# Kernel tuning notes

Measured on AMD Instinct MI355X. Metric: run time of the kernel, lower is better.

## Reference

```python
import jax, jax.numpy as jnp
import numpy as np

N_NODES = 20000
IN_CH = 512
HEADS = 8
CH = 64  # hidden_layer per head
E = 320000
E_LABEL = 100000


def setup_inputs() -> dict:
    key = jax.random.key(0)
    ks = jax.random.split(key, 8)
    x = jax.random.normal(ks[0], (N_NODES, IN_CH), dtype=jnp.float32)
    edge_index = jax.random.randint(ks[1], (2, E), 0, N_NODES)
    edge_label_index = jax.random.randint(ks[2], (2, E_LABEL), 0, N_NODES)
    # GATv2Conv params (share_weights=False, bias=True)
    sc = 1.0 / np.sqrt(IN_CH)
    W_l = jax.random.normal(ks[3], (IN_CH, HEADS * CH), dtype=jnp.float32) * sc
    W_r = jax.random.normal(ks[4], (IN_CH, HEADS * CH), dtype=jnp.float32) * sc
    att = jax.random.normal(ks[5], (HEADS, CH), dtype=jnp.float32) * (1.0 / np.sqrt(CH))
    bias = jnp.zeros((HEADS * CH,), dtype=jnp.float32)
    gamma = jnp.ones((HEADS * CH,), dtype=jnp.float32)
    beta = jnp.zeros((HEADS * CH,), dtype=jnp.float32)
    return {"x": x, "edge_index": edge_index, "edge_label_index": edge_label_index,
            "W_l": W_l, "W_r": W_r, "att": att, "bias": bias,
            "gamma": gamma, "beta": beta}


def reference(x, edge_index, edge_label_index, W_l, W_r, att, bias, gamma, beta):
    N = x.shape[0]
    H, C = att.shape
    src, dst = edge_index[0], edge_index[1]
    # GATv2Conv: separate source/target linear maps
    xl = (x @ W_l).reshape(N, H, C)
    xr = (x @ W_r).reshape(N, H, C)
    # per-edge attention logits (GATv2: leaky_relu BEFORE attention vector)
    e = jax.nn.leaky_relu(xl[src] + xr[dst], negative_slope=0.2)  # [E,H,C]
    alpha = jnp.einsum('ehc,hc->eh', e, att)                      # [E,H]
    # softmax over incoming edges of each destination node
    amax = jax.ops.segment_max(alpha, dst, num_segments=N)        # [N,H]
    alpha = jnp.exp(alpha - amax[dst])
    denom = jax.ops.segment_sum(alpha, dst, num_segments=N)       # [N,H]
    alpha = alpha / (denom[dst] + 1e-16)
    # scatter-add aggregation of attended source messages
    out = jax.ops.segment_sum(alpha[:, :, None] * xl[src], dst, num_segments=N)  # [N,H,C]
    out = out.reshape(N, H * C) + bias
    # BatchNorm1d (training-mode batch stats, eps=1e-5)
    mu = out.mean(axis=0)
    var = out.var(axis=0)
    out = (out - mu) * jax.lax.rsqrt(var + 1e-5) * gamma + beta
    out = jax.nn.relu(out)  # dropout is identity in deterministic reference
    # gather + dot-product link scoring
    s = out[edge_label_index[0]]
    t = out[edge_label_index[1]]
    return jnp.sum(s * t, axis=1)  # [E_LABEL]
```

## Files before the change

### kernel.cpp

```cpp
#include <hip/hip_runtime.h>
#include <hip/hip_bf16.h>
#include <cstdint>

#define IN_CH 512
#define HC    512
#define HEADS 8
#define NPACK 1024

typedef __attribute__((ext_vector_type(8))) short bf16x8;
typedef __attribute__((ext_vector_type(8))) ushort u16x8;
typedef __attribute__((ext_vector_type(4))) float f32x4;
typedef __attribute__((ext_vector_type(2))) float f32x2;
typedef const __attribute__((address_space(1))) uint8_t* gaddr_t;
typedef __attribute__((address_space(3))) uint8_t* laddr_t;

__device__ inline ushort f2bf(float f) {
  uint32_t u = __float_as_uint(f);
  return (ushort)((u + 0x7fffu + ((u >> 16) & 1u)) >> 16);
}
__device__ inline float bf2f(ushort u) {
  return __uint_as_float(((uint32_t)u) << 16);
}

#if defined(__has_builtin)
#if __has_builtin(__builtin_amdgcn_cvt_pk_f32_fp8) && __has_builtin(__builtin_amdgcn_cvt_pk_fp8_f32)
#define HAVE_HW_FP8 1
#endif
#if __has_builtin(__builtin_elementwise_max)
#define HAVE_EW_MAX 1
#endif
#endif

__device__ __forceinline__ float fp8_decode_sw(uint32_t v) {
  const uint32_t t = v & 0x7fu;
  float m;
  if (t >= 8u) m = __uint_as_float((((t >> 3) + 120u) << 23) | ((t & 7u) << 20));
  else m = (float)t * 0.001953125f;
  return (v & 0x80u) ? -m : m;
}
__device__ __forceinline__ uint8_t fp8_encode_sw(float f) {
  const uint32_t b = __float_as_uint(f);
  const uint32_t s = (b >> 24) & 0x80u;
  uint32_t a = b & 0x7fffffffu;
  if (a >= 0x43e00000u) return (uint8_t)(s | 0x7eu);
  if (a < 0x3c800000u) {
    const int qi = (int)(__uint_as_float(a) * 512.0f + 0.5f);
    return (uint8_t)(s | (qi >= 8 ? 8u : (uint32_t)qi));
  }
  const uint32_t r = a + 0x7ffffu + ((a >> 20) & 1u);
  const uint32_t e = r >> 23;
  if (e > 135u) return (uint8_t)(s | 0x7eu);
  return (uint8_t)(s | ((e - 120u) << 3) | ((r >> 20) & 7u));
}

template<bool HI>
__device__ __forceinline__ f32x2 fp8x2_dec(uint32_t u) {
#ifdef HAVE_HW_FP8
  return __builtin_amdgcn_cvt_pk_f32_fp8(u, HI);
#else
  const uint32_t w = HI ? (u >> 16) : u;
  f32x2 r;
  r.x = fp8_decode_sw(w & 0xffu);
  r.y = fp8_decode_sw((w >> 8) & 0xffu);
  return r;
#endif
}
__device__ __forceinline__ uint8_t f32_to_fp8(float f) {
#ifdef HAVE_HW_FP8
  return (uint8_t)(__builtin_amdgcn_cvt_pk_fp8_f32(f, f, 0, false) & 0xff);
#else
  return fp8_encode_sw(f);
#endif
}
__device__ __forceinline__ uint32_t fp8x4_pack(f32x2 a, f32x2 b) {
#ifdef HAVE_HW_FP8
  uint32_t w = __builtin_amdgcn_cvt_pk_fp8_f32(a.x, a.y, 0, false);
  w = __builtin_amdgcn_cvt_pk_fp8_f32(b.x, b.y, w, true);
  return w;
#else
  return (uint32_t)fp8_encode_sw(a.x) | ((uint32_t)fp8_encode_sw(a.y) << 8) |
         ((uint32_t)fp8_encode_sw(b.x) << 16) | ((uint32_t)fp8_encode_sw(b.y) << 24);
#endif
}

__device__ __forceinline__ f32x2 pk_max(f32x2 a, f32x2 b) {
#ifdef HAVE_EW_MAX
  return __builtin_elementwise_max(a, b);
#else
  f32x2 r; r.x = fmaxf(a.x, b.x); r.y = fmaxf(a.y, b.y); return r;
#endif
}

template<int CTRL>
__device__ __forceinline__ float dpp_add(float s) {
  const int t = __builtin_amdgcn_update_dpp(0, __float_as_int(s), CTRL, 0xf, 0xf, true);
  return s + __int_as_float(t);
}

__global__ void prep(const float* __restrict__ x, ushort* __restrict__ xb,
                     const float* __restrict__ Wl, const float* __restrict__ Wr,
                     ushort* __restrict__ bt,
                     const int* __restrict__ ei, int* __restrict__ counts,
                     const int* __restrict__ eli, int* __restrict__ counts2,
                     int n4, int E, int EL, int nbc, int nbp, int nbh) {
  const int b = blockIdx.x;
  if (b < nbc) {
    const int i = b * 256 + threadIdx.x;
    if (i < n4) {
      const float4 v = ((const float4*)x)[i];
      ushort4 o;
      o.x = f2bf(v.x); o.y = f2bf(v.y); o.z = f2bf(v.z); o.w = f2bf(v.w);
      ((ushort4*)xb)[i] = o;
    }
  } else if (b < nbc + nbp) {
    const int i = (b - nbc) * 256 + threadIdx.x;
    if (i < NPACK * IN_CH) {
      const int n = i >> 9, k = i & 511;
      const float v = (n < HC) ? Wl[(size_t)k * HC + n] : Wr[(size_t)k * HC + (n - HC)];
      bt[i] = f2bf(v);
    }
  } else if (b < nbc + nbp + nbh) {
    const int e = (b - nbc - nbp) * 256 + threadIdx.x;
    if (e < E) atomicAdd(&counts[ei[E + e]], 1);
  } else {
    const int e = (b - nbc - nbp - nbh) * 256 + threadIdx.x;
    if (e < EL) atomicAdd(&counts2[eli[e]], 1);
  }
}

__global__ __launch_bounds__(512) void gemm_mfma(
    const ushort* __restrict__ xb, const ushort* __restrict__ bt,
    uint8_t* __restrict__ xl8, ushort* __restrict__ xrb, int M) {
  __shared__ __align__(16) ushort As[3][256 * 32];
  __shared__ __align__(16) ushort Bs[3][128 * 32];
  const int sw  = (blockIdx.x & 7) * 79 + (blockIdx.x >> 3);
  const int row0 = (sw >> 3) * 256;
  const int col0 = (sw & 7) * 128;
  const int wave = threadIdx.x >> 6, lane = threadIdx.x & 63;
  const int quad = lane >> 4, m16 = lane & 15;
  const int wrow = (wave >> 1) * 64;
  const int wcol = (wave & 1) * 64;
  const int srow = lane >> 2;
  const int scol = (lane & 3) * 8;
  const f32x4 zero = {0.f, 0.f, 0.f, 0.f};
  f32x4 acc[4][4];
  #pragma unroll
  for (int i = 0; i < 4; ++i)
    #pragma unroll
    for (int j = 0; j < 4; ++j) acc[i][j] = zero;

  auto stage = [&](int buf, int kt) {
    const int k0 = kt * 32;
    const int r = wave * 16 + srow;
    const ushort* ga0 = xb + (size_t)(row0 + r) * IN_CH + k0 + scol;
    __builtin_amdgcn_global_load_lds((gaddr_t)ga0, (laddr_t)(&As[buf][(wave * 16) * 32]), 16, 0, 0);
    const ushort* ga1 = xb + (size_t)(row0 + 128 + r) * IN_CH + k0 + scol;
    __builtin_amdgcn_global_load_lds((gaddr_t)ga1, (laddr_t)(&As[buf][(128 + wave * 16) * 32]), 16, 0, 0);
    const ushort* gb = bt + (size_t)(col0 + r) * IN_CH + k0 + scol;
    __builtin_amdgcn_global_load_lds((gaddr_t)gb, (laddr_t)(&Bs[buf][(wave * 16) * 32]), 16, 0, 0);
  };
  auto compute = [&](int buf) {
    bf16x8 af[4], bfr[4];
    #pragma unroll
    for (int i = 0; i < 4; ++i)
      af[i] = *(const bf16x8*)(&As[buf][(wrow + i * 16 + m16) * 32 + quad * 8]);
    #pragma unroll
    for (int j = 0; j < 4; ++j)
      bfr[j] = *(const bf16x8*)(&Bs[buf][(wcol + j * 16 + m16) * 32 + quad * 8]);
    #pragma unroll
    for (int i = 0; i < 4; ++i)
      #pragma unroll
      for (int j = 0; j < 4; ++j)
        acc[i][j] = __builtin_amdgcn_mfma_f32_16x16x32_bf16(af[i], bfr[j], acc[i][j], 0, 0, 0);
  };

  stage(0, 0);
  stage(1, 1);
  int buf = 0;
  for (int kt = 0; kt <= 13; ++kt) {
    asm volatile("s_waitcnt vmcnt(3)" ::: "memory");
    __builtin_amdgcn_s_barrier();
    int nbuf = buf + 2; if (nbuf >= 3) nbuf -= 3;
    stage(nbuf, kt + 2);
    compute(buf);
    ++buf; if (buf == 3) buf = 0;
  }
  asm volatile("s_waitcnt vmcnt(3)" ::: "memory");
  __builtin_amdgcn_s_barrier();
  compute(buf);
  ++buf; if (buf == 3) buf = 0;
  asm volatile("s_waitcnt vmcnt(0)" ::: "memory");
  __builtin_amdgcn_s_barrier();
  compute(buf);

  const bool isL = (col0 < HC);
  if (isL) {
    #pragma unroll
    for (int i = 0; i < 4; ++i) {
      const int r = row0 + wrow + i * 16 + quad * 4;
      #pragma unroll
      for (int j = 0; j < 4; ++j) {
        const int cg = col0 + wcol + j * 16 + m16;
        #pragma unroll
        for (int t = 0; t < 4; ++t) {
          const int rr = r + t;
          if (rr < M) xl8[(size_t)rr * HC + cg] = f32_to_fp8(acc[i][j][t]);
        }
      }
    }
  } else {
    const int cbase = col0 - HC;
    #pragma unroll
    for (int i = 0; i < 4; ++i) {
      const int r = row0 + wrow + i * 16 + quad * 4;
      #pragma unroll
      for (int j = 0; j < 4; ++j) {
        const int cg = cbase + wcol + j * 16 + m16;
        #pragma unroll
        for (int t = 0; t < 4; ++t) {
          const int rr = r + t;
          if (rr < M) xrb[(size_t)rr * HC + cg] = f2bf(acc[i][j][t]);
        }
      }
    }
  }
}

__global__ __launch_bounds__(256) void scan_fused(
    const int* __restrict__ cA, int* __restrict__ oA, int* __restrict__ curA,
    int* __restrict__ fA,
    const int* __restrict__ cB, int* __restrict__ oB, int* __restrict__ curB,
    int* __restrict__ fB, int Nn, int nb) {
  const int half = (blockIdx.x >= nb) ? 1 : 0;
  const int blk  = blockIdx.x - half * nb;
  const int* counts = half ? cB : cA;
  int* offsets = half ? oB : oA;
  int* cursor  = half ? curB : curA;
  int* flags   = half ? fB : fA;
  __shared__ int tmp[256];
  __shared__ int sPref;
  const int t = threadIdx.x;
  const int i = blk * 256 + t;
  const int v = (i < Nn) ? counts[i] : 0;
  tmp[t] = v;
  __syncthreads();
  for (int d = 1; d < 256; d <<= 1) {
    int add = (t >= d) ? tmp[t - d] : 0;
    __syncthreads();
    tmp[t] += add;
    __syncthreads();
  }
  if (t == 0) atomicExch(&flags[blk], tmp[255] + 1);
  if (t < 64) {
    int s = 0;
    for (int b = t; b < blk; b += 64) {
      int f;
      do { f = atomicOr(&flags[b], 0); } while (f == 0);
      s += f - 1;
    }
    #pragma unroll
    for (int off = 32; off > 0; off >>= 1) s += __shfl_down(s, off, 64);
    if (t == 0) sPref = s;
  }
  __syncthreads();
  const int pref = sPref;
  if (i < Nn) {
    const int o = tmp[t] - v + pref;
    offsets[i] = o;
    cursor[i] = o;
  }
}

__global__ void csr_fill(const int* __restrict__ ei, int* __restrict__ cursor,
                         int* __restrict__ csr_src,
                         const int* __restrict__ eli, int* __restrict__ cursor2,
                         int2* __restrict__ csr_te, int E, int EL, int nbE) {
  const int b = blockIdx.x;
  if (b < nbE) {
    const int e = b * 256 + threadIdx.x;
    if (e < E) {
      const int pos = atomicAdd(&cursor[ei[E + e]], 1);
      csr_src[pos] = ei[e];
    }
  } else {
    const int e = (b - nbE) * 256 + threadIdx.x;
    if (e < EL) {
      const int pos = atomicAdd(&cursor2[eli[e]], 1);
      csr_te[pos] = make_int2(eli[EL + e], e);
    }
  }
}

__global__ __launch_bounds__(256) void gatv2_agg(
    const uint8_t* __restrict__ xl8, const ushort* xrb, const float* __restrict__ att,
    const int* __restrict__ offsets, const int* __restrict__ counts,
    const int* __restrict__ csr_src, uint8_t* __restrict__ agg8, int Nn) {
  const int node = blockIdx.x * 4 + (threadIdx.x >> 6);
  const int lane = threadIdx.x & 63;
  if (node >= Nn) return;
  const int start = offsets[node];
  const int deg   = counts[node];
  uint2* pd = (uint2*)(agg8 + (size_t)node * HC + lane * 8);
  if (deg == 0) {
    const uint2 z = {0u, 0u};
    *pd = z;
    return;
  }
  f32x2 rv2[4], tv2[4];
  {
    const u16x8 ur = *(const u16x8*)(xrb + (size_t)node * HC + lane * 8);
    #pragma unroll
    for (int c = 0; c < 4; ++c) {
      rv2[c].x = bf2f((ushort)ur[2 * c]);
      rv2[c].y = bf2f((ushort)ur[2 * c + 1]);
    }
    const float4* pa = (const float4*)(att + lane * 8);
    const float4 t0 = pa[0], t1 = pa[1];
    tv2[0].x = t0.x; tv2[0].y = t0.y;
    tv2[1].x = t0.z; tv2[1].y = t0.w;
    tv2[2].x = t1.x; tv2[2].y = t1.y;
    tv2[3].x = t1.z; tv2[3].y = t1.w;
  }
  f32x2 acc2[4] = {{0.f, 0.f}, {0.f, 0.f}, {0.f, 0.f}, {0.f, 0.f}};
  float densum = 0.f;
  const int* ps = csr_src + start;
  auto row = [&](int idx) {
    return *(const uint2*)(xl8 + (size_t)ps[idx] * HC + lane * 8);
  };
  auto body = [&](const uint2 cur) {
    f32x2 a0 = fp8x2_dec<false>(cur.x);
    f32x2 a1 = fp8x2_dec<true>(cur.x);
    f32x2 a2 = fp8x2_dec<false>(cur.y);
    f32x2 a3 = fp8x2_dec<true>(cur.y);
    f32x2 v, s2;
    v = a0 + rv2[0]; s2  = pk_max(v, 0.2f * v) * tv2[0];
    v = a1 + rv2[1]; s2 += pk_max(v, 0.2f * v) * tv2[1];
    v = a2 + rv2[2]; s2 += pk_max(v, 0.2f * v) * tv2[2];
    v = a3 + rv2[3]; s2 += pk_max(v, 0.2f * v) * tv2[3];
    float s = s2.x + s2.y;
    s = dpp_add<0xB1>(s);
    s = dpp_add<0x4E>(s);
    s = dpp_add<0x141>(s);
    const float ea = __expf(s);
    densum += ea;
    const f32x2 eav = {ea, ea};
    acc2[0] += eav * a0;
    acc2[1] += eav * a1;
    acc2[2] += eav * a2;
    acc2[3] += eav * a3;
  };

  uint2 b0 = {}, b1 = {};
  b0 = row(0);
  if (deg > 1) b1 = row(1);
  int i = 0;
  for (; i + 2 <= deg; i += 2) {
    const uint2 c0 = b0;
    if (i + 2 < deg) b0 = row(i + 2);
    const uint2 c1 = b1;
    if (i + 3 < deg) b1 = row(i + 3);
    body(c0);
    body(c1);
  }
  if (i < deg) body(b0);

  const float inv = 1.0f / (densum + 1e-16f);
  const f32x2 iv = {inv, inv};
  uint2 pack;
  pack.x = fp8x4_pack(acc2[0] * iv, acc2[1] * iv);
  pack.y = fp8x4_pack(acc2[2] * iv, acc2[3] * iv);
  *pd = pack;
}

__global__ void bn_stats(const uint8_t* __restrict__ agg8, float* __restrict__ gsum,
                         float* __restrict__ gsq, int* __restrict__ ctr,
                         const float* __restrict__ gamma, const float* __restrict__ beta,
                         float* __restrict__ aScale, float* __restrict__ bShift,
                         float invN, int Nn) {
  const int t = threadIdx.x;
  const int rows_per_block = (Nn + gridDim.x - 1) / gridDim.x;
  const int r0 = blockIdx.x * rows_per_block;
  const int r1 = min(Nn, r0 + rows_per_block);
  float s0 = 0.f, s1 = 0.f, q0 = 0.f, q1 = 0.f;
  for (int r = r0; r < r1; ++r) {
    const uchar2 u = ((const uchar2*)(agg8 + (size_t)r * HC))[t];
    const f32x2 v = fp8x2_dec<false>((uint32_t)u.x | ((uint32_t)u.y << 8));
    s0 += v.x; q0 += v.x * v.x;
    s1 += v.y; q1 += v.y * v.y;
  }
  atomicAdd(&gsum[2 * t], s0);
  atomicAdd(&gsum[2 * t + 1], s1);
  atomicAdd(&gsq[2 * t], q0);
  atomicAdd(&gsq[2 * t + 1], q1);
  __shared__ int isLast;
  __syncthreads();
  if (t == 0) {
    __threadfence();
    isLast = (atomicAdd(ctr, 1) == (int)gridDim.x - 1) ? 1 : 0;
  }
  __syncthreads();
  if (isLast) {
    #pragma unroll
    for (int k = 0; k < 2; ++k) {
      const int c = t + k * 256;
      const float sum = atomicAdd(&gsum[c], 0.0f);
      const float sq  = atomicAdd(&gsq[c], 0.0f);
      const float m = sum * invN;
      const float var = sq * invN - m * m;
      const float rs = rsqrtf(var + 1e-5f);
      const float a = rs * gamma[c];
      aScale[c] = a;
      bShift[c] = beta[c] - m * a;
    }
  }
}

__global__ __launch_bounds__(256) void score_g(
    const uint8_t* __restrict__ agg8, const float* __restrict__ aScale,
    const float* __restrict__ bShift, const int* __restrict__ off2,
    const int* __restrict__ cnt2, const int2* __restrict__ csr_te,
    float* __restrict__ out, int Nn) {
  const int node = blockIdx.x * 4 + (threadIdx.x >> 6);
  const int lane = threadIdx.x & 63;
  if (node >= Nn) return;
  const int start = off2[node];
  const int deg   = cnt2[node];
  if (deg == 0) return;
  const f32x2 z2 = {0.f, 0.f};
  f32x2 aS2[4], bS2[4], ys2[4];
  {
    const float4* pa = (const float4*)(aScale + lane * 8);
    const float4 a0 = pa[0], a1 = pa[1];
    aS2[0].x=a0.x; aS2[0].y=a0.y; aS2[1].x=a0.z; aS2[1].y=a0.w;
    aS2[2].x=a1.x; aS2[2].y=a1.y; aS2[3].x=a1.z; aS2[3].y=a1.w;
    const float4* pb = (const float4*)(bShift + lane * 8);
    const float4 c0 = pb[0], c1 = pb[1];
    bS2[0].x=c0.x; bS2[0].y=c0.y; bS2[1].x=c0.z; bS2[1].y=c0.w;
    bS2[2].x=c1.x; bS2[2].y=c1.y; bS2[3].x=c1.z; bS2[3].y=c1.w;
    const uint2 us = *(const uint2*)(agg8 + (size_t)node * HC + lane * 8);
    ys2[0] = pk_max(z2, fp8x2_dec<false>(us.x) * aS2[0] + bS2[0]);
    ys2[1] = pk_max(z2, fp8x2_dec<true>(us.x)  * aS2[1] + bS2[1]);
    ys2[2] = pk_max(z2, fp8x2_dec<false>(us.y) * aS2[2] + bS2[2]);
    ys2[3] = pk_max(z2, fp8x2_dec<true>(us.y)  * aS2[3] + bS2[3]);
  }
  const int2* pte = csr_te + start;
  auto row = [&](int idx) {
    return *(const uint2*)(agg8 + (size_t)pte[idx].x * HC + lane * 8);
  };
  auto emit = [&](const uint2 ut, int eid) {
    f32x2 s2;
    s2  = ys2[0] * pk_max(z2, fp8x2_dec<false>(ut.x) * aS2[0] + bS2[0]);
    s2 += ys2[1] * pk_max(z2, fp8x2_dec<true>(ut.x)  * aS2[1] + bS2[1]);
    s2 += ys2[2] * pk_max(z2, fp8x2_dec<false>(ut.y) * aS2[2] + bS2[2]);
    s2 += ys2[3] * pk_max(z2, fp8x2_dec<true>(ut.y)  * aS2[3] + bS2[3]);
    float s = s2.x + s2.y;
    s = dpp_add<0xB1>(s);
    s = dpp_add<0x4E>(s);
    s = dpp_add<0x141>(s);
    s = dpp_add<0x140>(s);
    s = dpp_add<0x142>(s);
    s = dpp_add<0x143>(s);
    if (lane == 63) out[eid] = s;
  };
  uint2 b0 = {}, b1 = {};
  b0 = row(0);
  if (deg > 1) b1 = row(1);
  int j = 0;
  for (; j + 2 <= deg; j += 2) {
    const uint2 c0 = b0;
    if (j + 2 < deg) b0 = row(j + 2);
    const uint2 c1 = b1;
    if (j + 3 < deg) b1 = row(j + 3);
    emit(c0, pte[j].y);
    emit(c1, pte[j + 1].y);
  }
  if (j < deg) emit(b0, pte[j].y);
}

extern "C" void kernel_launch(void* const* d_in, const int* in_sizes, int n_in,
                              void* d_out, int out_size, void* d_ws, size_t ws_size,
                              hipStream_t stream) {
  const float* x     = (const float*)d_in[0];
  const int*   ei    = (const int*)d_in[1];
  const int*   eli   = (const int*)d_in[2];
  const float* W_l   = (const float*)d_in[3];
  const float* W_r   = (const float*)d_in[4];
  const float* att   = (const float*)d_in[5];
  const float* gamma = (const float*)d_in[7];
  const float* beta  = (const float*)d_in[8];
  float* out = (float*)d_out;

  const int Nn = in_sizes[0] / IN_CH;
  const int E  = in_sizes[1] / 2;
  const int EL = in_sizes[2] / 2;

  uint8_t* xl8 = (uint8_t*)d_ws;
  ushort* xrb = (ushort*)d_ws + (size_t)Nn * HC;
  ushort* xbf = xrb + (size_t)Nn * HC;
  ushort* btb = xbf + (size_t)Nn * IN_CH;
  int* counts   = (int*)(btb + (size_t)NPACK * IN_CH);
  int* counts2  = counts + Nn;
  float* gsum   = (float*)(counts2 + Nn);
  float* gsq    = gsum + HC;
  int* flagsA   = (int*)(gsq + HC);
  int* flagsB   = flagsA + 128;
  int* bnctr    = flagsB + 128;
  int* offsets  = bnctr + 64;
  int* cursor   = offsets + Nn;
  int* offsets2 = cursor + Nn;
  int* cursor2  = offsets2 + Nn;
  int* csr_src  = cursor2 + Nn;
  int2* csr_te  = (int2*)(csr_src + E);
  float* aScale = (float*)(csr_te + EL);
  float* bShift = aScale + HC;
  uint8_t* agg8 = (uint8_t*)xbf;

  const int nb  = (Nn + 255) / 256;
  const int nbc = (Nn * IN_CH / 4 + 255) / 256;
  const int nbp = (NPACK * IN_CH + 255) / 256;
  const int nbh = (E + 255) / 256;
  const int nbh2 = (EL + 255) / 256;

  (void)hipMemsetAsync(counts, 0, (2 * (size_t)Nn + 2 * HC + 320) * sizeof(int), stream);

  prep<<<nbc + nbp + nbh + nbh2, 256, 0, stream>>>(
      x, xbf, W_l, W_r, btb, ei, counts, eli, counts2,
      Nn * IN_CH / 4, E, EL, nbc, nbp, nbh);

  gemm_mfma<<<632, 512, 0, stream>>>(xbf, btb, xl8, xrb, Nn);

  scan_fused<<<2 * nb, 256, 0, stream>>>(counts, offsets, cursor, flagsA,
                                         counts2, offsets2, cursor2, flagsB, Nn, nb);
  csr_fill<<<nbh + nbh2, 256, 0, stream>>>(ei, cursor, csr_src,
                                           eli, cursor2, csr_te, E, EL, nbh);

  gatv2_agg<<<(Nn + 3) / 4, 256, 0, stream>>>(xl8, xrb, att, offsets, counts,
                                              csr_src, agg8, Nn);

  bn_stats<<<200, 256, 0, stream>>>(agg8, gsum, gsq, bnctr, gamma, beta,
                                    aScale, bShift, 1.0f / (float)Nn, Nn);

  score_g<<<(Nn + 3) / 4, 256, 0, stream>>>(agg8, aScale, bShift, offsets2,
                                            counts2, csr_te, out, Nn);
}
```

Measured before the change: 271.2 us.

## Fuse BatchNorm statistics accumulation into GATv2 aggregation kernel

Removes the separate bn_stats launch and computes per-channel sum and sum-of-squares inside gatv2_agg. Each block reduces its four nodes into shared memory with atomics, then issues 1024 global float atomics, and a last-block counter finalizes the scale and shift. This saves one kernel launch and a reread of agg8. In exchange it adds about 5000 blocks each doing 1024 global atomics on the same 1024 addresses, which can create heavy contention. It also changes the statistics to use the unquantized values rather than the fp8-decoded ones.

```diff
diff --git a/kernel.cpp b/kernel.cpp
--- a/kernel.cpp
+++ b/kernel.cpp
@@ -294,107 +294,115 @@
 __global__ __launch_bounds__(256) void gatv2_agg(
     const uint8_t* __restrict__ xl8, const ushort* xrb, const float* __restrict__ att,
     const int* __restrict__ offsets, const int* __restrict__ counts,
-    const int* __restrict__ csr_src, uint8_t* __restrict__ agg8, int Nn) {
+    const int* __restrict__ csr_src, uint8_t* __restrict__ agg8,
+    float* __restrict__ gsum, float* __restrict__ gsq, int* __restrict__ ctr,
+    const float* __restrict__ gamma, const float* __restrict__ beta,
+    float* __restrict__ aScale, float* __restrict__ bShift, float invN, int Nn) {
+  __shared__ float sSum[HC];
+  __shared__ float sSq[HC];
   const int node = blockIdx.x * 4 + (threadIdx.x >> 6);
   const int lane = threadIdx.x & 63;
-  if (node >= Nn) return;
-  const int start = offsets[node];
-  const int deg   = counts[node];
-  uint2* pd = (uint2*)(agg8 + (size_t)node * HC + lane * 8);
-  if (deg == 0) {
-    const uint2 z = {0u, 0u};
-    *pd = z;
-    return;
-  }
-  f32x2 rv2[4], tv2[4];
-  {
-    const u16x8 ur = *(const u16x8*)(xrb + (size_t)node * HC + lane * 8);
-    #pragma unroll
-    for (int c = 0; c < 4; ++c) {
-      rv2[c].x = bf2f((ushort)ur[2 * c]);
-      rv2[c].y = bf2f((ushort)ur[2 * c + 1]);
-    }
-    const float4* pa = (const float4*)(att + lane * 8);
-    const float4 t0 = pa[0], t1 = pa[1];
-    tv2[0].x = t0.x; tv2[0].y = t0.y;
-    tv2[1].x = t0.z; tv2[1].y = t0.w;
-    tv2[2].x = t1.x; tv2[2].y = t1.y;
-    tv2[3].x = t1.z; tv2[3].y = t1.w;
-  }
-  f32x2 acc2[4] = {{0.f, 0.f}, {0.f, 0.f}, {0.f, 0.f}, {0.f, 0.f}};
-  float densum = 0.f;
-  const int* ps = csr_src + start;
-  auto row = [&](int idx) {
-    return *(const uint2*)(xl8 + (size_t)ps[idx] * HC + lane * 8);
-  };
-  auto body = [&](const uint2 cur) {
-    f32x2 a0 = fp8x2_dec<false>(cur.x);
-    f32x2 a1 = fp8x2_dec<true>(cur.x);
-    f32x2 a2 = fp8x2_dec<false>(cur.y);
-    f32x2 a3 = fp8x2_dec<true>(cur.y);
-    f32x2 v, s2;
-    v = a0 + rv2[0]; s2  = pk_max(v, 0.2f * v) * tv2[0];
-    v = a1 + rv2[1]; s2 += pk_max(v, 0.2f * v) * tv2[1];
-    v = a2 + rv2[2]; s2 += pk_max(v, 0.2f * v) * tv2[2];
-    v = a3 + rv2[3]; s2 += pk_max(v, 0.2f * v) * tv2[3];
-    float s = s2.x + s2.y;
-    s = dpp_add<0xB1>(s);
-    s = dpp_add<0x4E>(s);
-    s = dpp_add<0x141>(s);
-    const float ea = __expf(s);
-    densum += ea;
-    const f32x2 eav = {ea, ea};
-    acc2[0] += eav * a0;
-    acc2[1] += eav * a1;
-    acc2[2] += eav * a2;
-    acc2[3] += eav * a3;
-  };
-
-  uint2 b0 = {}, b1 = {};
-  b0 = row(0);
-  if (deg > 1) b1 = row(1);
-  int i = 0;
-  for (; i + 2 <= deg; i += 2) {
-    const uint2 c0 = b0;
-    if (i + 2 < deg) b0 = row(i + 2);
-    const uint2 c1 = b1;
-    if (i + 3 < deg) b1 = row(i + 3);
-    body(c0);
-    body(c1);
-  }
-  if (i < deg) body(b0);
-
-  const float inv = 1.0f / (densum + 1e-16f);
-  const f32x2 iv = {inv, inv};
-  uint2 pack;
-  pack.x = fp8x4_pack(acc2[0] * iv, acc2[1] * iv);
-  pack.y = fp8x4_pack(acc2[2] * iv, acc2[3] * iv);
-  *pd = pack;
-}
-
-__global__ void bn_stats(const uint8_t* __restrict__ agg8, float* __restrict__ gsum,
-                         float* __restrict__ gsq, int* __restrict__ ctr,
-                         const float* __restrict__ gamma, const float* __restrict__ beta,
-                         float* __restrict__ aScale, float* __restrict__ bShift,
-                         float invN, int Nn) {
-  const int t = threadIdx.x;
-  const int rows_per_block = (Nn + gridDim.x - 1) / gridDim.x;
-  const int r0 = blockIdx.x * rows_per_block;
-  const int r1 = min(Nn, r0 + rows_per_block);
-  float s0 = 0.f, s1 = 0.f, q0 = 0.f, q1 = 0.f;
-  for (int r = r0; r < r1; ++r) {
-    const uchar2 u = ((const uchar2*)(agg8 + (size_t)r * HC))[t];
-    const f32x2 v = fp8x2_dec<false>((uint32_t)u.x | ((uint32_t)u.y << 8));
-    s0 += v.x; q0 += v.x * v.x;
-    s1 += v.y; q1 += v.y * v.y;
-  }
-  atomicAdd(&gsum[2 * t], s0);
-  atomicAdd(&gsum[2 * t + 1], s1);
-  atomicAdd(&gsq[2 * t], q0);
-  atomicAdd(&gsq[2 * t + 1], q1);
+  const int tid  = threadIdx.x;
+  sSum[tid] = 0.f; sSum[tid + 256] = 0.f;
+  sSq[tid]  = 0.f; sSq[tid + 256]  = 0.f;
+
+  f32x2 v2[4] = {{0.f, 0.f}, {0.f, 0.f}, {0.f, 0.f}, {0.f, 0.f}};
+  const bool active = (node < Nn);
+  if (active) {
+    const int start = offsets[node];
+    const int deg   = counts[node];
+    uint2* pd = (uint2*)(agg8 + (size_t)node * HC + lane * 8);
+    if (deg == 0) {
+      const uint2 z = {0u, 0u};
+      *pd = z;
+    } else {
+      f32x2 rv2[4], tv2[4];
+      {
+        const u16x8 ur = *(const u16x8*)(xrb + (size_t)node * HC + lane * 8);
+        #pragma unroll
+        for (int c = 0; c < 4; ++c) {
+          rv2[c].x = bf2f((ushort)ur[2 * c]);
+          rv2[c].y = bf2f((ushort)ur[2 * c + 1]);
+        }
+        const float4* pa = (const float4*)(att + lane * 8);
+        const float4 t0 = pa[0], t1 = pa[1];
+        tv2[0].x = t0.x; tv2[0].y = t0.y;
+        tv2[1].x = t0.z; tv2[1].y = t0.w;
+        tv2[2].x = t1.x; tv2[2].y = t1.y;
+        tv2[3].x = t1.z; tv2[3].y = t1.w;
+      }
+      f32x2 acc2[4] = {{0.f, 0.f}, {0.f, 0.f}, {0.f, 0.f}, {0.f, 0.f}};
+      float densum = 0.f;
+      const int* ps = csr_src + start;
+      auto row = [&](int idx) {
+        return *(const uint2*)(xl8 + (size_t)ps[idx] * HC + lane * 8);
+      };
+      auto body = [&](const uint2 cur) {
+        f32x2 a0 = fp8x2_dec<false>(cur.x);
+        f32x2 a1 = fp8x2_dec<true>(cur.x);
+        f32x2 a2 = fp8x2_dec<false>(cur.y);
+        f32x2 a3 = fp8x2_dec<true>(cur.y);
+        f32x2 v, s2;
+        v = a0 + rv2[0]; s2  = pk_max(v, 0.2f * v) * tv2[0];
+        v = a1 + rv2[1]; s2 += pk_max(v, 0.2f * v) * tv2[1];
+        v = a2 + rv2[2]; s2 += pk_max(v, 0.2f * v) * tv2[2];
+        v = a3 + rv2[3]; s2 += pk_max(v, 0.2f * v) * tv2[3];
+        float s = s2.x + s2.y;
+        s = dpp_add<0xB1>(s);
+        s = dpp_add<0x4E>(s);
+        s = dpp_add<0x141>(s);
+        const float ea = __expf(s);
+        densum += ea;
+        const f32x2 eav = {ea, ea};
+        acc2[0] += eav * a0;
+        acc2[1] += eav * a1;
+        acc2[2] += eav * a2;
+        acc2[3] += eav * a3;
+      };
+
+      uint2 b0 = {}, b1 = {};
+      b0 = row(0);
+      if (deg > 1) b1 = row(1);
+      int i = 0;
+      for (; i + 2 <= deg; i += 2) {
+        const uint2 c0 = b0;
+        if (i + 2 < deg) b0 = row(i + 2);
+        const uint2 c1 = b1;
+        if (i + 3 < deg) b1 = row(i + 3);
+        body(c0);
+        body(c1);
+      }
+      if (i < deg) body(b0);
+
+      const float inv = 1.0f / (densum + 1e-16f);
+      const f32x2 iv = {inv, inv};
+      v2[0] = acc2[0] * iv; v2[1] = acc2[1] * iv;
+      v2[2] = acc2[2] * iv; v2[3] = acc2[3] * iv;
+      uint2 pack;
+      pack.x = fp8x4_pack(v2[0], v2[1]);
+      pack.y = fp8x4_pack(v2[2], v2[3]);
+      *pd = pack;
+    }
+  }
+  __syncthreads();
+  if (active) {
+    #pragma unroll
+    for (int p = 0; p < 4; ++p) {
+      const int ch = lane * 8 + 2 * p;
+      atomicAdd(&sSum[ch],     v2[p].x);
+      atomicAdd(&sSum[ch + 1], v2[p].y);
+      atomicAdd(&sSq[ch],      v2[p].x * v2[p].x);
+      atomicAdd(&sSq[ch + 1],  v2[p].y * v2[p].y);
+    }
+  }
+  __syncthreads();
+  atomicAdd(&gsum[tid],       sSum[tid]);
+  atomicAdd(&gsum[tid + 256], sSum[tid + 256]);
+  atomicAdd(&gsq[tid],        sSq[tid]);
+  atomicAdd(&gsq[tid + 256],  sSq[tid + 256]);
   __shared__ int isLast;
   __syncthreads();
-  if (t == 0) {
+  if (tid == 0) {
     __threadfence();
     isLast = (atomicAdd(ctr, 1) == (int)gridDim.x - 1) ? 1 : 0;
   }
@@ -402,7 +410,7 @@
   if (isLast) {
     #pragma unroll
     for (int k = 0; k < 2; ++k) {
-      const int c = t + k * 256;
+      const int c = tid + k * 256;
       const float sum = atomicAdd(&gsum[c], 0.0f);
       const float sq  = atomicAdd(&gsq[c], 0.0f);
       const float m = sum * invN;
@@ -535,10 +543,9 @@
                                            eli, cursor2, csr_te, E, EL, nbh);
 
   gatv2_agg<<<(Nn + 3) / 4, 256, 0, stream>>>(xl8, xrb, att, offsets, counts,
-                                              csr_src, agg8, Nn);
-
-  bn_stats<<<200, 256, 0, stream>>>(agg8, gsum, gsq, bnctr, gamma, beta,
-                                    aScale, bShift, 1.0f / (float)Nn, Nn);
+                                              csr_src, agg8, gsum, gsq, bnctr,
+                                              gamma, beta, aScale, bShift,
+                                              1.0f / (float)Nn, Nn);
 
   score_g<<<(Nn + 3) / 4, 256, 0, stream>>>(agg8, aScale, bShift, offsets2,
                                             counts2, csr_te, out, Nn);
```

Result: slower. 375.4 us (+38.4%).

## Use BK=64 GEMM tiles with XOR-swizzled LDS and split-phase staging

Applied to the files above, without the earlier changes.

The MFMA GEMM moves from a 32-wide to a 64-wide K tile, halving the main-loop iterations to 8. LDS rows are XOR-swizzled to avoid bank conflicts on the fragment reads. Global-to-LDS staging for the next buffer is spread across two sub-steps, and s_setprio raises wave priority around the MFMA bursts. LDS use doubles to about 144KB per block, which may limit occupancy, and the vmcnt bookkeeping becomes more fragile.

```diff
diff --git a/kernel.cpp b/kernel.cpp
--- a/kernel.cpp
+++ b/kernel.cpp
@@ -131,76 +131,100 @@
 __global__ __launch_bounds__(512) void gemm_mfma(
     const ushort* __restrict__ xb, const ushort* __restrict__ bt,
     uint8_t* __restrict__ xl8, ushort* __restrict__ xrb, int M) {
-  __shared__ __align__(16) ushort As[3][256 * 32];
-  __shared__ __align__(16) ushort Bs[3][128 * 32];
+  __shared__ __align__(16) ushort As[3][256 * 64];
+  __shared__ __align__(16) ushort Bs[3][128 * 64];
   const int sw  = (blockIdx.x & 7) * 79 + (blockIdx.x >> 3);
   const int row0 = (sw >> 3) * 256;
   const int col0 = (sw & 7) * 128;
   const int wave = threadIdx.x >> 6, lane = threadIdx.x & 63;
   const int quad = lane >> 4, m16 = lane & 15;
-  const int wrow = (wave >> 1) * 64;
-  const int wcol = (wave & 1) * 64;
-  const int srow = lane >> 2;
-  const int scol = (lane & 3) * 8;
-  const f32x4 zero = {0.f, 0.f, 0.f, 0.f};
+  const int wm = wave >> 1;
+  const int wn = wave & 1;
   f32x4 acc[4][4];
   #pragma unroll
   for (int i = 0; i < 4; ++i)
     #pragma unroll
-    for (int j = 0; j < 4; ++j) acc[i][j] = zero;
-
-  auto stage = [&](int buf, int kt) {
-    const int k0 = kt * 32;
-    const int r = wave * 16 + srow;
-    const ushort* ga0 = xb + (size_t)(row0 + r) * IN_CH + k0 + scol;
-    __builtin_amdgcn_global_load_lds((gaddr_t)ga0, (laddr_t)(&As[buf][(wave * 16) * 32]), 16, 0, 0);
-    const ushort* ga1 = xb + (size_t)(row0 + 128 + r) * IN_CH + k0 + scol;
-    __builtin_amdgcn_global_load_lds((gaddr_t)ga1, (laddr_t)(&As[buf][(128 + wave * 16) * 32]), 16, 0, 0);
-    const ushort* gb = bt + (size_t)(col0 + r) * IN_CH + k0 + scol;
-    __builtin_amdgcn_global_load_lds((gaddr_t)gb, (laddr_t)(&Bs[buf][(wave * 16) * 32]), 16, 0, 0);
-  };
-  auto compute = [&](int buf) {
-    bf16x8 af[4], bfr[4];
-    #pragma unroll
-    for (int i = 0; i < 4; ++i)
-      af[i] = *(const bf16x8*)(&As[buf][(wrow + i * 16 + m16) * 32 + quad * 8]);
-    #pragma unroll
-    for (int j = 0; j < 4; ++j)
-      bfr[j] = *(const bf16x8*)(&Bs[buf][(wcol + j * 16 + m16) * 32 + quad * 8]);
-    #pragma unroll
-    for (int i = 0; i < 4; ++i)
-      #pragma unroll
-      for (int j = 0; j < 4; ++j)
-        acc[i][j] = __builtin_amdgcn_mfma_f32_16x16x32_bf16(af[i], bfr[j], acc[i][j], 0, 0, 0);
-  };
-
-  stage(0, 0);
-  stage(1, 1);
+    for (int j = 0; j < 4; ++j) acc[i][j] = {0.f, 0.f, 0.f, 0.f};
+
+  auto stage = [&](int buf, int kt, int c) {
+    #pragma unroll
+    for (int ld = 0; ld < 2; ++ld) {
+      const int s = (wave + ld * 8) * 64 + lane;
+      const int r = s >> 3, sl = s & 7;
+      const int srcK = kt * 64 + ((sl ^ (r & 7)) << 3);
+      if (c < 2) {
+        const ushort* g = xb + (size_t)(row0 + c * 128 + r) * IN_CH + srcK;
+        __builtin_amdgcn_global_load_lds((gaddr_t)g,
+            (laddr_t)(&As[buf][c * 8192 + s * 8]), 16, 0, 0);
+      } else {
+        const ushort* g = bt + (size_t)(col0 + r) * IN_CH + srcK;
+        __builtin_amdgcn_global_load_lds((gaddr_t)g,
+            (laddr_t)(&Bs[buf][s * 8]), 16, 0, 0);
+      }
+    }
+  };
+  auto rdA = [&](int buf, int i, int ks) {
+    const int R = wm * 64 + i * 16 + m16;
+    const int slot = (ks * 4 + quad) ^ (R & 7);
+    return *(const bf16x8*)(&As[buf][R * 64 + slot * 8]);
+  };
+  auto rdB = [&](int buf, int j, int ks) {
+    const int C = wn * 64 + j * 16 + m16;
+    const int slot = (ks * 4 + quad) ^ (C & 7);
+    return *(const bf16x8*)(&Bs[buf][C * 64 + slot * 8]);
+  };
+
+  stage(0, 0, 0); stage(0, 0, 1); stage(0, 0, 2);
+  stage(1, 1, 0); stage(1, 1, 1); stage(1, 1, 2);
+
   int buf = 0;
-  for (int kt = 0; kt <= 13; ++kt) {
-    asm volatile("s_waitcnt vmcnt(3)" ::: "memory");
+  for (int kt = 0; kt < 8; ++kt) {
+    if (kt < 7) { asm volatile("s_waitcnt vmcnt(6)" ::: "memory"); }
+    else        { asm volatile("s_waitcnt vmcnt(0)" ::: "memory"); }
     __builtin_amdgcn_s_barrier();
     int nbuf = buf + 2; if (nbuf >= 3) nbuf -= 3;
-    stage(nbuf, kt + 2);
-    compute(buf);
+    {
+      bf16x8 af[4], bfr[4];
+      #pragma unroll
+      for (int i = 0; i < 4; ++i) af[i] = rdA(buf, i, 0);
+      #pragma unroll
+      for (int j = 0; j < 4; ++j) bfr[j] = rdB(buf, j, 0);
+      if (kt < 6) { stage(nbuf, kt + 2, 0); stage(nbuf, kt + 2, 1); }
+      __builtin_amdgcn_s_setprio(1);
+      #pragma unroll
+      for (int i = 0; i < 4; ++i)
+        #pragma unroll
+        for (int j = 0; j < 4; ++j)
+          acc[i][j] = __builtin_amdgcn_mfma_f32_16x16x32_bf16(af[i], bfr[j], acc[i][j], 0, 0, 0);
+      __builtin_amdgcn_s_setprio(0);
+    }
+    __builtin_amdgcn_s_barrier();
+    {
+      bf16x8 af[4], bfr[4];
+      #pragma unroll
+      for (int i = 0; i < 4; ++i) af[i] = rdA(buf, i, 1);
+      #pragma unroll
+      for (int j = 0; j < 4; ++j) bfr[j] = rdB(buf, j, 1);
+      if (kt < 6) stage(nbuf, kt + 2, 2);
+      __builtin_amdgcn_s_setprio(1);
+      #pragma unroll
+      for (int i = 0; i < 4; ++i)
+        #pragma unroll
+        for (int j = 0; j < 4; ++j)
+          acc[i][j] = __builtin_amdgcn_mfma_f32_16x16x32_bf16(af[i], bfr[j], acc[i][j], 0, 0, 0);
+      __builtin_amdgcn_s_setprio(0);
+    }
     ++buf; if (buf == 3) buf = 0;
   }
-  asm volatile("s_waitcnt vmcnt(3)" ::: "memory");
-  __builtin_amdgcn_s_barrier();
-  compute(buf);
-  ++buf; if (buf == 3) buf = 0;
-  asm volatile("s_waitcnt vmcnt(0)" ::: "memory");
-  __builtin_amdgcn_s_barrier();
-  compute(buf);
 
   const bool isL = (col0 < HC);
   if (isL) {
     #pragma unroll
     for (int i = 0; i < 4; ++i) {
-      const int r = row0 + wrow + i * 16 + quad * 4;
+      const int r = row0 + wm * 64 + i * 16 + quad * 4;
       #pragma unroll
       for (int j = 0; j < 4; ++j) {
-        const int cg = col0 + wcol + j * 16 + m16;
+        const int cg = col0 + wn * 64 + j * 16 + m16;
         #pragma unroll
         for (int t = 0; t < 4; ++t) {
           const int rr = r + t;
@@ -212,10 +236,10 @@
     const int cbase = col0 - HC;
     #pragma unroll
     for (int i = 0; i < 4; ++i) {
-      const int r = row0 + wrow + i * 16 + quad * 4;
+      const int r = row0 + wm * 64 + i * 16 + quad * 4;
       #pragma unroll
       for (int j = 0; j < 4; ++j) {
-        const int cg = cbase + wcol + j * 16 + m16;
+        const int cg = cbase + wn * 64 + j * 16 + m16;
         #pragma unroll
         for (int t = 0; t < 4; ++t) {
           const int rr = r + t;
```

After: 273.0 us. About the same (+0.7%).
